# Performance work log

Hardware: AMD Instinct MI355X
Metric: run time of the kernel (lower is better)

## Reference

```python
import jax, jax.numpy as jnp
import numpy as np

NUM_HEADS = 8
NS = 27  # 3x3x3 deformable samples per query


def _resize1d(x, axis, new):
    # linear resize along one axis, align_corners=False (matches F.interpolate); identity if size matches
    old = x.shape[axis]
    if old == new:
        return x
    pos = (jnp.arange(new, dtype=jnp.float32) + 0.5) * (old / new) - 0.5
    f = jnp.floor(pos)
    w = pos - f
    i0 = jnp.clip(f, 0, old - 1).astype(jnp.int32)
    i1 = jnp.clip(f + 1, 0, old - 1).astype(jnp.int32)
    shp = [1] * x.ndim
    shp[axis] = new
    w = w.reshape(shp)
    return jnp.take(x, i0, axis=axis) * (1 - w) + jnp.take(x, i1, axis=axis) * w


def _rel_to_abs(x):
    # x: (b, d, h, w, w+NS-1) -> (b, d, h, w, NS) via the pad/reshape shifting trick
    b, d, h, w, c = x.shape
    x = jnp.pad(x, ((0, 0), (0, 0), (0, 0), (0, 0), (0, 1)))
    x = x.reshape(b, d, h, w * (c + 1))
    x = jnp.pad(x, ((0, 0), (0, 0), (0, 0), (0, NS - 1)))
    x = x.reshape(b, d, h, w + 1, NS + w - 1)
    return x[:, :, :, :w, w - 1:]


def _rel_logits_1d(q, rel_k):
    # q: (BH, 1, A, B, C, hd); rel_k: (C+NS-1, hd) -> (BH, A, B, C, NS)
    logits = jnp.einsum('nzxywd,rd->nzxywr', q, rel_k)
    n, z, a, b, c, r = logits.shape
    return _rel_to_abs(logits.reshape(n, z * a, b, c, r))


def _pos_emb(q, rel_depth, rel_height, rel_width, D, H, W):
    # q: (BH, 1, D, H, W, hd) -> (BH, D, H, W, NS)
    rw = _resize1d(rel_width, 0, W + NS - 1)
    rh = _resize1d(rel_height, 0, H + NS - 1)
    rd = _resize1d(rel_depth, 0, D + NS - 1)
    lw = _rel_logits_1d(q, rw)            # (BH, D, H, W, NS)
    qh = jnp.swapaxes(q, 3, 4)            # (BH, 1, D, W, H, hd)
    lh = _rel_logits_1d(qh, rh)           # (BH, D, W, H, NS)
    qd = jnp.swapaxes(qh, 2, 4)           # (BH, 1, H, W, D, hd)
    ld = _rel_logits_1d(qd, rd)           # (BH, H, W, D, NS)
    # trilinear resize of lh/ld to (D, H, W) over spatial axes (identity when D==H==W)
    for ax, tgt in ((1, D), (2, H), (3, W)):
        lh = _resize1d(lh, ax, tgt)
        ld = _resize1d(ld, ax, tgt)
    return lw + lh + ld


def _deform_unfold3d(x, offset):
    # x: (BH, C, D, H, W); offset: (BH, NS*3, D, H, W) -> (BH, C*NS, D*H*W)
    BH, C, D, H, W = x.shape
    off = offset.reshape(BH, NS, 3, D, H, W)
    k = jnp.arange(NS)
    kz = (k // 9 - 1).astype(jnp.float32)
    ky = (k // 3 % 3 - 1).astype(jnp.float32)
    kx = (k % 3 - 1).astype(jnp.float32)
    zz, yy, xx = jnp.meshgrid(jnp.arange(D, dtype=jnp.float32),
                              jnp.arange(H, dtype=jnp.float32),
                              jnp.arange(W, dtype=jnp.float32), indexing='ij')
    pz = zz + kz[:, None, None, None] + off[:, :, 0]   # (BH, NS, D, H, W)
    py = yy + ky[:, None, None, None] + off[:, :, 1]
    px = xx + kx[:, None, None, None] + off[:, :, 2]
    z0 = jnp.floor(pz); y0 = jnp.floor(py); x0 = jnp.floor(px)
    wz = pz - z0; wy = py - y0; wx = px - x0
    z0 = z0.astype(jnp.int32); y0 = y0.astype(jnp.int32); x0 = x0.astype(jnp.int32)
    S = D * H * W
    xf = x.reshape(BH, C, S)
    acc = jnp.zeros((BH, C, NS * S), dtype=x.dtype)
    for dz in (0, 1):
        for dy in (0, 1):
            for dx in (0, 1):
                zi = z0 + dz; yi = y0 + dy; xi = x0 + dx
                valid = ((zi >= 0) & (zi < D) & (yi >= 0) & (yi < H) & (xi >= 0) & (xi < W)).astype(x.dtype)
                w = (wz if dz else 1 - wz) * (wy if dy else 1 - wy) * (wx if dx else 1 - wx) * valid
                idx = (jnp.clip(zi, 0, D - 1) * H + jnp.clip(yi, 0, H - 1)) * W + jnp.clip(xi, 0, W - 1)
                g = jnp.take_along_axis(xf, idx.reshape(BH, 1, NS * S), axis=2)  # (BH, C, NS*S)
                acc = acc + g * w.reshape(BH, 1, NS * S)
    return acc.reshape(BH, C * NS, S)


def _forward(x, w_qkv, w_proj, b_proj, w_off, rel_depth, rel_height, rel_width, D, H, W):
    B, N, C = x.shape
    nh = NUM_HEADS
    hd = C // nh
    scale = hd ** -0.5
    BH = B * nh
    qkv = (x @ w_qkv.T).reshape(B, N, 3, nh, hd)
    q = qkv[:, :, 0].transpose(0, 2, 1, 3)  # (B, nh, N, hd)
    k = qkv[:, :, 1].transpose(0, 2, 1, 3)
    v = qkv[:, :, 2].transpose(0, 2, 1, 3)
    offset = (x.reshape(B, N, nh, hd) @ w_off.T).transpose(0, 2, 3, 1).reshape(BH, NS * 3, D, H, W)
    kmap = k.transpose(0, 1, 3, 2).reshape(BH, hd, D, H, W)
    vmap = v.transpose(0, 1, 3, 2).reshape(BH, hd, D, H, W)
    ks = _deform_unfold3d(kmap, offset).transpose(0, 2, 1).reshape(B, nh, N, hd, NS)
    vs = _deform_unfold3d(vmap, offset).reshape(B, nh, hd, NS, N).transpose(0, 1, 4, 3, 2)  # (B, nh, N, NS, hd)
    attn = jnp.einsum('bhnd,bhnds->bhns', q, ks) * scale
    pos = _pos_emb(q.reshape(BH, 1, D, H, W, hd), rel_depth, rel_height, rel_width, D, H, W).reshape(B, nh, N, NS)
    attn = jax.nn.softmax(attn + pos, axis=-1)
    out = jnp.einsum('bhns,bhnsd->bhnd', attn, vs).transpose(0, 2, 1, 3).reshape(B, N, C)
    return out @ w_proj.T + b_proj


def setup_inputs():
    key = jax.random.key(0)
    ks = jax.random.split(key, 8)
    B, D, H, W, C = 1, 16, 16, 16, 512
    N = D * H * W
    hd = C // NUM_HEADS
    return {
        'x': jax.random.normal(ks[0], (B, N, C), dtype=jnp.float32),
        'w_qkv': jax.random.normal(ks[1], (3 * C, C), dtype=jnp.float32) * 0.02,
        'w_proj': jax.random.normal(ks[2], (C, C), dtype=jnp.float32) * 0.02,
        'b_proj': jnp.zeros((C,), dtype=jnp.float32),
        'w_off': jax.random.normal(ks[3], (NS * 3, hd), dtype=jnp.float32) * 0.01,
        'rel_depth': jax.random.normal(ks[4], (D + NS - 1, hd), dtype=jnp.float32) * hd ** -0.5,
        'rel_height': jax.random.normal(ks[5], (H + NS - 1, hd), dtype=jnp.float32) * hd ** -0.5,
        'rel_width': jax.random.normal(ks[6], (W + NS - 1, hd), dtype=jnp.float32) * hd ** -0.5,
        'D': D, 'H': H, 'W': W,
    }


def reference(x, w_qkv, w_proj, b_proj, w_off, rel_depth, rel_height, rel_width, D, H, W):
    return _forward(x, w_qkv, w_proj, b_proj, w_off, rel_depth, rel_height, rel_width, D, H, W)
```

## Files before the change

kernel.cpp:

```cpp
#include <hip/hip_runtime.h>
#include <hip/hip_fp16.h>
#include <math.h>
#include <stdint.h>

#define NH    8
#define HD    64
#define NTOK  4096
#define CDIM  512
#define NSAMP 27

typedef __attribute__((ext_vector_type(8))) _Float16 half8;
typedef __attribute__((ext_vector_type(4))) float floatx4;
typedef unsigned short ushort_t;

__device__ __forceinline__ ushort_t f16b(float f) {
  return __half_as_ushort(__float2half(f));
}
__device__ __forceinline__ __half2 u2h2(uint32_t u) { return __builtin_bit_cast(__half2, u); }
__device__ __forceinline__ uint32_t h22u(__half2 h) { return __builtin_bit_cast(uint32_t, h); }

__device__ __forceinline__ float wave_sum_bcast(float x) {
#define DPP_STEP(ctrl, rmask)                                                   \
  { int t = __builtin_amdgcn_update_dpp(0, __float_as_int(x), ctrl, rmask, 0xf, \
                                        true);                                  \
    x += __int_as_float(t); }
  DPP_STEP(0x111, 0xf)
  DPP_STEP(0x112, 0xf)
  DPP_STEP(0x114, 0xf)
  DPP_STEP(0x118, 0xf)
  DPP_STEP(0x142, 0xa)
  DPP_STEP(0x143, 0xc)
#undef DPP_STEP
  return __int_as_float(__builtin_amdgcn_readlane(__float_as_int(x), 63));
}

__global__ __launch_bounds__(256) void k_cvt(const float* __restrict__ x,
                                             const float* __restrict__ wq,
                                             const float* __restrict__ wp,
                                             const float* __restrict__ w_off,
                                             const float* __restrict__ rel_d,
                                             const float* __restrict__ rel_h,
                                             const float* __restrict__ rel_w,
                                             ushort_t* __restrict__ xb,
                                             ushort_t* __restrict__ wqb,
                                             ushort_t* __restrict__ wpb,
                                             ushort_t* __restrict__ w_offh,
                                             ushort_t* __restrict__ relh) {
  int i = blockIdx.x * 256 + threadIdx.x;
  const float4* src = nullptr;
  ushort_t* dst;
  int off;
  float4 v = make_float4(0.f, 0.f, 0.f, 0.f);
  if (i < 524288)      { src = (const float4*)x;  dst = xb;  off = i; }
  else if (i < 720896) { src = (const float4*)wq; dst = wqb; off = i - 524288; }
  else if (i < 786432) { src = (const float4*)wp; dst = wpb; off = i - 720896; }
  else {
    int t = i - 786432;
    if (t < 2048) {
      off = t;
      int e = t * 4, row = e >> 6;
      if (row < 81) v = *(const float4*)&w_off[e];
      dst = w_offh;
    } else {
      off = t - 2048;
      int e = off * 4, row = e >> 6, col = e & 63;
      if (row < 42)       v = *(const float4*)&rel_w[row * 64 + col];
      else if (row < 84)  v = *(const float4*)&rel_h[(row - 42) * 64 + col];
      else if (row < 126) v = *(const float4*)&rel_d[(row - 84) * 64 + col];
      dst = relh;
    }
  }
  if (src) v = src[off];
  ushort4 o = make_ushort4(f16b(v.x), f16b(v.y), f16b(v.z), f16b(v.w));
  *(ushort4*)&dst[(size_t)off * 4] = o;
}

__global__ __launch_bounds__(256) void k_qkv(const ushort_t* __restrict__ Ah,
                                             const ushort_t* __restrict__ Bth,
                                             ushort_t* __restrict__ qh16,
                                             uint32_t* __restrict__ kvb) {
  __shared__ __align__(16) ushort_t As[128 * 32];
  __shared__ __align__(16) ushort_t Bs[128 * 32];
  __shared__ __align__(16) ushort_t Cs[128 * 136];
  const int tid = threadIdx.x;
  const int wave = tid >> 6, lane = tid & 63;
  const int wr = wave >> 1, wc = wave & 1;
  const int m15 = lane & 15, quad = lane >> 4;
  const int bm = blockIdx.x, bn = blockIdx.y;
  const bool is_q = (bn < 4);
  const int h = bn - 4;
  floatx4 acc[4][4];
#pragma unroll
  for (int i = 0; i < 4; i++)
#pragma unroll
    for (int j = 0; j < 4; j++) acc[i][j] = {0.f, 0.f, 0.f, 0.f};

  const int r0 = tid >> 2, c0 = (tid & 3) * 8;
  const int r1 = r0 + 64;
  const int brA = is_q ? (bn * 128 + r0) : (512 + h * 64 + r0);
  const int brB = is_q ? (bn * 128 + r1) : (1024 + h * 64 + r0);
  for (int k0 = 0; k0 < 512; k0 += 32) {
    *(uint4*)&As[r0 * 32 + c0] = *(const uint4*)&Ah[(size_t)(bm * 128 + r0) * 512 + k0 + c0];
    *(uint4*)&As[r1 * 32 + c0] = *(const uint4*)&Ah[(size_t)(bm * 128 + r1) * 512 + k0 + c0];
    *(uint4*)&Bs[r0 * 32 + c0] = *(const uint4*)&Bth[(size_t)brA * 512 + k0 + c0];
    *(uint4*)&Bs[r1 * 32 + c0] = *(const uint4*)&Bth[(size_t)brB * 512 + k0 + c0];
    __syncthreads();
    half8 af[4], bf[4];
#pragma unroll
    for (int i = 0; i < 4; i++)
      af[i] = *(const half8*)&As[(wr * 64 + i * 16 + m15) * 32 + quad * 8];
#pragma unroll
    for (int j = 0; j < 4; j++)
      bf[j] = *(const half8*)&Bs[(wc * 64 + j * 16 + m15) * 32 + quad * 8];
#pragma unroll
    for (int i = 0; i < 4; i++)
#pragma unroll
      for (int j = 0; j < 4; j++)
        acc[i][j] = __builtin_amdgcn_mfma_f32_16x16x32_f16(af[i], bf[j], acc[i][j], 0, 0, 0);
    __syncthreads();
  }

#pragma unroll
  for (int i = 0; i < 4; i++)
#pragma unroll
    for (int j = 0; j < 4; j++) {
      int col = wc * 64 + j * 16 + m15;
#pragma unroll
      for (int r = 0; r < 4; r++) {
        int row = wr * 64 + i * 16 + quad * 4 + r;
        Cs[row * 136 + col] = f16b(acc[i][j][r]);
      }
    }
  __syncthreads();

  if (is_q) {
#pragma unroll
    for (int it = 0; it < 8; it++) {
      int id = it * 256 + tid;
      int hh = id >> 10, row = (id >> 3) & 127, chunk = id & 7;
      uint4 d = *(const uint4*)&Cs[row * 136 + hh * 64 + chunk * 8];
      int hq = bn * 2 + hh;
      *(uint4*)&qh16[((size_t)hq * NTOK + bm * 128 + row) * 64 + chunk * 8] = d;
    }
  } else {
#pragma unroll
    for (int it = 0; it < 8; it++) {
      int id = it * 256 + tid;
      int row = id >> 4, chunk = id & 15;
      uint2 kk = *(const uint2*)&Cs[row * 136 + chunk * 4];
      uint2 vv = *(const uint2*)&Cs[row * 136 + 64 + chunk * 4];
      uint4 o;
      o.x = (kk.x & 0xffffu) | (vv.x << 16);
      o.y = (kk.x >> 16) | (vv.x & 0xffff0000u);
      o.z = (kk.y & 0xffffu) | (vv.y << 16);
      o.w = (kk.y >> 16) | (vv.y & 0xffff0000u);
      *(uint4*)&kvb[((size_t)h * NTOK + bm * 128 + row) * 64 + chunk * 4] = o;
    }
  }
}

__global__ __launch_bounds__(256) void k_aux(const ushort_t* __restrict__ xh,
                                             const ushort_t* __restrict__ qh16,
                                             const ushort_t* __restrict__ w_offh,
                                             const ushort_t* __restrict__ relh,
                                             float* __restrict__ ob,
                                             float* __restrict__ Pb) {
  __shared__ __align__(16) ushort_t As[128 * 32];
  __shared__ __align__(16) ushort_t Bs[128 * 32];
  const int tid = threadIdx.x;
  const int wave = tid >> 6, lane = tid & 63;
  const int wr = wave >> 1, wc = wave & 1;
  const int m15 = lane & 15, quad = lane >> 4;
  const int bm = blockIdx.x;
  const int mode = blockIdx.y >> 3, h = blockIdx.y & 7;

  const ushort_t* A;  int lda;
  const ushort_t* B;
  float* C;  int NC;
  if (mode == 0) { A = xh + h * 64;                  lda = 512; B = w_offh; C = ob + (size_t)h * NTOK * 81;  NC = 81; }
  else           { A = qh16 + (size_t)h * NTOK * 64; lda = 64;  B = relh;   C = Pb + (size_t)h * NTOK * 126; NC = 126; }

  floatx4 acc[4][4];
#pragma unroll
  for (int i = 0; i < 4; i++)
#pragma unroll
    for (int j = 0; j < 4; j++) acc[i][j] = {0.f, 0.f, 0.f, 0.f};

  const int r0 = tid >> 2, c0 = (tid & 3) * 8;
  const int r1 = r0 + 64;
  for (int k0 = 0; k0 < 64; k0 += 32) {
    *(uint4*)&As[r0 * 32 + c0] = *(const uint4*)&A[(size_t)(bm * 128 + r0) * lda + k0 + c0];
    *(uint4*)&As[r1 * 32 + c0] = *(const uint4*)&A[(size_t)(bm * 128 + r1) * lda + k0 + c0];
    *(uint4*)&Bs[r0 * 32 + c0] = *(const uint4*)&B[(size_t)r0 * 64 + k0 + c0];
    *(uint4*)&Bs[r1 * 32 + c0] = *(const uint4*)&B[(size_t)r1 * 64 + k0 + c0];
    __syncthreads();
    half8 af[4], bf[4];
#pragma unroll
    for (int i = 0; i < 4; i++)
      af[i] = *(const half8*)&As[(wr * 64 + i * 16 + m15) * 32 + quad * 8];
#pragma unroll
    for (int j = 0; j < 4; j++)
      bf[j] = *(const half8*)&Bs[(wc * 64 + j * 16 + m15) * 32 + quad * 8];
#pragma unroll
    for (int i = 0; i < 4; i++)
#pragma unroll
      for (int j = 0; j < 4; j++)
        acc[i][j] = __builtin_amdgcn_mfma_f32_16x16x32_f16(af[i], bf[j], acc[i][j], 0, 0, 0);
    __syncthreads();
  }

#pragma unroll
  for (int i = 0; i < 4; i++)
#pragma unroll
    for (int j = 0; j < 4; j++) {
      int col = wc * 64 + j * 16 + m15;
      if (col < NC) {
#pragma unroll
        for (int r = 0; r < 4; r++) {
          int row = bm * 128 + wr * 64 + i * 16 + quad * 4 + r;
          C[(size_t)row * NC + col] = acc[i][j][r];
        }
      }
    }
}

__global__ __launch_bounds__(256) void k_attn(const ushort_t* __restrict__ qh16,
                                              const uint32_t* __restrict__ kvb,
                                              const float* __restrict__ obuf,
                                              const float* __restrict__ Pbuf,
                                              ushort_t* __restrict__ attb16) {
  __shared__ int      s_off[4][NSAMP][8];
  __shared__ uint32_t s_cwh[4][NSAMP][8];
  __shared__ uint32_t vpair[4][14][64];
  __shared__ uint32_t s_wp[4][14];
  const int bid = blockIdx.x;
  const int h = bid & 7;
  const int wave = threadIdx.x >> 6;
  const int lane = threadIdx.x & 63;
  const int n = (bid >> 3) * 4 + wave;
  const int z = n >> 8, y = (n >> 4) & 15, xq = n & 15;
  const float qd = __half2float(__ushort_as_half(qh16[((size_t)h * NTOK + n) * 64 + lane]));
  const char* kvc = (const char*)(kvb + (size_t)h * NTOK * 64);
  const uint32_t lane4 = (uint32_t)lane * 4u;

  if (lane < NSAMP) {
    const int s = lane;
    const float* op = &obuf[((size_t)h * NTOK + n) * 81 + s * 3];
    float oz = op[0], oy = op[1], ox = op[2];
    float pz = (float)(z + (s / 9) - 1) + oz;
    float py = (float)(y + ((s / 3) % 3) - 1) + oy;
    float px = (float)(xq + (s % 3) - 1) + ox;
    float fz = floorf(pz), fy = floorf(py), fx = floorf(px);
    float wz = pz - fz, wy = py - fy, wx = px - fx;
    int z0 = (int)fz, y0 = (int)fy, x0 = (int)fx;
    int      oarr[8];
    uint32_t warr[8];
#pragma unroll
    for (int c = 0; c < 8; c++) {
      int dz = (c >> 2) & 1, dy = (c >> 1) & 1, dx = c & 1;
      int zi = z0 + dz, yi = y0 + dy, xi = x0 + dx;
      bool valid = (zi >= 0) && (zi < 16) && (yi >= 0) && (yi < 16) && (xi >= 0) && (xi < 16);
      float w = (dz ? wz : 1.f - wz) * (dy ? wy : 1.f - wy) * (dx ? wx : 1.f - wx);
      int zc = min(max(zi, 0), 15), yc = min(max(yi, 0), 15), xc = min(max(xi, 0), 15);
      oarr[c] = ((zc * 16 + yc) * 16 + xc) * 256;
      uint32_t hw = (uint32_t)f16b(valid ? w : 0.f);
      warr[c] = hw | (hw << 16);
    }
    *(int4*)&s_off[wave][s][0]  = make_int4(oarr[0], oarr[1], oarr[2], oarr[3]);
    *(int4*)&s_off[wave][s][4]  = make_int4(oarr[4], oarr[5], oarr[6], oarr[7]);
    *(uint4*)&s_cwh[wave][s][0] = make_uint4(warr[0], warr[1], warr[2], warr[3]);
    *(uint4*)&s_cwh[wave][s][4] = make_uint4(warr[4], warr[5], warr[6], warr[7]);
  }

  float mydot = 0.f;
  uint32_t prev_acc = 0;
#pragma unroll 2
  for (int s = 0; s < NSAMP; s++) {
    int4  o0 = *(const int4*)&s_off[wave][s][0];
    int4  o1 = *(const int4*)&s_off[wave][s][4];
    uint4 c0 = *(const uint4*)&s_cwh[wave][s][0];
    uint4 c1 = *(const uint4*)&s_cwh[wave][s][4];
    __half2 acc2 = u2h2(0u);
    uint32_t p;
#define CORNER(OV, WV)                                                       \
    p = *(const uint32_t*)(kvc + (uint32_t)((uint32_t)OV + lane4));          \
    acc2 = __hfma2(u2h2(WV), u2h2(p), acc2);
    CORNER(o0.x, c0.x) CORNER(o0.y, c0.y) CORNER(o0.z, c0.z) CORNER(o0.w, c0.w)
    CORNER(o1.x, c1.x) CORNER(o1.y, c1.y) CORNER(o1.z, c1.z) CORNER(o1.w, c1.w)
#undef CORNER
    float ak = __half2float(acc2.x);
    float tot = wave_sum_bcast(qd * ak);
    mydot = (lane == s) ? tot : mydot;
    uint32_t au = h22u(acc2);
    if (s & 1)
      vpair[wave][s >> 1][lane] = (prev_acc >> 16) | (au & 0xffff0000u);
    else
      prev_acc = au;
  }
  vpair[wave][13][lane] = prev_acc >> 16;

  float logit = -INFINITY;
  if (lane < NSAMP) {
    int j = 15 + lane - xq;
    int n2 = (z * 16 + xq) * 16 + y;
    int n3 = (xq * 16 + z) * 16 + y;
    float pos = Pbuf[((size_t)h * NTOK + n) * 126 + j]
              + Pbuf[((size_t)h * NTOK + n2) * 126 + 42 + j]
              + Pbuf[((size_t)h * NTOK + n3) * 126 + 84 + j];
    logit = mydot * 0.125f + pos;
  }

  float mx = logit;
#pragma unroll
  for (int off = 32; off >= 1; off >>= 1) mx = fmaxf(mx, __shfl_xor(mx, off, 64));
  float e = __expf(logit - mx);
  float sum = e;
#pragma unroll
  for (int off = 32; off >= 1; off >>= 1) sum += __shfl_xor(sum, off, 64);
  const float wgt = e / sum;
  uint32_t hw = (uint32_t)f16b(wgt);
  uint32_t nw = (uint32_t)__shfl_down((int)hw, 1, 64);
  if ((lane & 1) == 0 && lane < 28)
    s_wp[wave][lane >> 1] = hw | (nw << 16);

  __half2 out2 = u2h2(0u);
#pragma unroll
  for (int p2 = 0; p2 < 14; p2++) {
    __half2 v2 = u2h2(vpair[wave][p2][lane]);
    __half2 w2 = u2h2(s_wp[wave][p2]);
    out2 = __hfma2(w2, v2, out2);
  }
  float out = __half2float(out2.x) + __half2float(out2.y);
  attb16[(size_t)n * 512 + h * 64 + lane] = f16b(out);
}

__global__ __launch_bounds__(256) void k_proj(const ushort_t* __restrict__ Ah,
                                              const ushort_t* __restrict__ Bth,
                                              const float* __restrict__ bias,
                                              float* __restrict__ out) {
  __shared__ __align__(16) ushort_t As[128 * 32];
  __shared__ __align__(16) ushort_t Bs[128 * 32];
  const int tid = threadIdx.x;
  const int wave = tid >> 6, lane = tid & 63;
  const int wr = wave >> 1, wc = wave & 1;
  const int m15 = lane & 15, quad = lane >> 4;
  const int bm = blockIdx.x, bn = blockIdx.y;
  floatx4 acc[4][4];
#pragma unroll
  for (int i = 0; i < 4; i++)
#pragma unroll
    for (int j = 0; j < 4; j++) acc[i][j] = {0.f, 0.f, 0.f, 0.f};

  const int r0 = tid >> 2, c0 = (tid & 3) * 8;
  const int r1 = r0 + 64;
  for (int k0 = 0; k0 < 512; k0 += 32) {
    *(uint4*)&As[r0 * 32 + c0] = *(const uint4*)&Ah[(size_t)(bm * 128 + r0) * 512 + k0 + c0];
    *(uint4*)&As[r1 * 32 + c0] = *(const uint4*)&Ah[(size_t)(bm * 128 + r1) * 512 + k0 + c0];
    *(uint4*)&Bs[r0 * 32 + c0] = *(const uint4*)&Bth[(size_t)(bn * 128 + r0) * 512 + k0 + c0];
    *(uint4*)&Bs[r1 * 32 + c0] = *(const uint4*)&Bth[(size_t)(bn * 128 + r1) * 512 + k0 + c0];
    __syncthreads();
    half8 af[4], bf[4];
#pragma unroll
    for (int i = 0; i < 4; i++)
      af[i] = *(const half8*)&As[(wr * 64 + i * 16 + m15) * 32 + quad * 8];
#pragma unroll
    for (int j = 0; j < 4; j++)
      bf[j] = *(const half8*)&Bs[(wc * 64 + j * 16 + m15) * 32 + quad * 8];
#pragma unroll
    for (int i = 0; i < 4; i++)
#pragma unroll
      for (int j = 0; j < 4; j++)
        acc[i][j] = __builtin_amdgcn_mfma_f32_16x16x32_f16(af[i], bf[j], acc[i][j], 0, 0, 0);
    __syncthreads();
  }

#pragma unroll
  for (int i = 0; i < 4; i++)
#pragma unroll
    for (int j = 0; j < 4; j++) {
      int col = bn * 128 + wc * 64 + j * 16 + m15;
      float b = bias[col];
#pragma unroll
      for (int r = 0; r < 4; r++) {
        int row = bm * 128 + wr * 64 + i * 16 + quad * 4 + r;
        out[(size_t)row * 512 + col] = acc[i][j][r] + b;
      }
    }
}

extern "C" void kernel_launch(void* const* d_in, const int* in_sizes, int n_in,
                              void* d_out, int out_size, void* d_ws, size_t ws_size,
                              hipStream_t stream) {
  const float* x      = (const float*)d_in[0];
  const float* w_qkv  = (const float*)d_in[1];
  const float* w_proj = (const float*)d_in[2];
  const float* b_proj = (const float*)d_in[3];
  const float* w_off  = (const float*)d_in[4];
  const float* rel_d  = (const float*)d_in[5];
  const float* rel_h  = (const float*)d_in[6];
  const float* rel_w  = (const float*)d_in[7];

  char* ws = (char*)d_ws;
  uint32_t* kvb    = (uint32_t*)ws; ws += (size_t)NH * NTOK * 64 * 4;
  float*    ob     = (float*)ws;    ws += (size_t)NH * NTOK * 81 * 4;
  float*    Pb     = (float*)ws;    ws += (size_t)NH * NTOK * 126 * 4;
  ushort_t* attb16 = (ushort_t*)ws; ws += (size_t)NTOK * CDIM * 2;
  ushort_t* xh     = (ushort_t*)ws; ws += (size_t)NTOK * CDIM * 2;
  ushort_t* wqh    = (ushort_t*)ws; ws += (size_t)3 * CDIM * CDIM * 2;
  ushort_t* wph    = (ushort_t*)ws; ws += (size_t)CDIM * CDIM * 2;
  ushort_t* qh16   = (ushort_t*)ws; ws += (size_t)NH * NTOK * 64 * 2;
  ushort_t* w_offh = (ushort_t*)ws; ws += (size_t)128 * 64 * 2;
  ushort_t* relh   = (ushort_t*)ws; ws += (size_t)128 * 64 * 2;
  float*    out    = (float*)d_out;

  k_cvt <<<dim3(3088), dim3(256), 0, stream>>>(x, w_qkv, w_proj, w_off, rel_d, rel_h,
                                               rel_w, xh, wqh, wph, w_offh, relh);
  k_qkv <<<dim3(32, 12), dim3(256), 0, stream>>>(xh, wqh, qh16, kvb);
  k_aux <<<dim3(32, 16), dim3(256), 0, stream>>>(xh, qh16, w_offh, relh, ob, Pb);
  k_attn<<<dim3(8192),   dim3(256), 0, stream>>>(qh16, kvb, ob, Pb, attb16);
  k_proj<<<dim3(32, 4),  dim3(256), 0, stream>>>(attb16, wph, b_proj, out);
}
```

Measured before the change: 181.6 us.

## Fold offset and relative-position projections into the QKV GEMM via precomposed weights

Precomputes block-diagonal offset weights and rel-embedding×Wq composite weights so the offset and positional logits come straight from x. They are computed in one larger merged GEMM launch alongside QKV, and the separate aux kernel that depended on q is removed. This drops one dependent launch and lets the small GEMMs share the QKV grid. In exchange the offset and rel GEMMs now use K=512 instead of 64, which adds MFMA work and weight traffic. The composite weights are rounded to fp16 after an fp32 product, which changes numerics slightly.

After: 194.6 us. +7.2%, slower.

```diff
diff --git a/kernel.cpp b/kernel.cpp
--- a/kernel.cpp
+++ b/kernel.cpp
@@ -34,51 +34,73 @@
   return __int_as_float(__builtin_amdgcn_readlane(__float_as_int(x), 63));
 }
 
-__global__ __launch_bounds__(256) void k_cvt(const float* __restrict__ x,
-                                             const float* __restrict__ wq,
-                                             const float* __restrict__ wp,
-                                             const float* __restrict__ w_off,
-                                             const float* __restrict__ rel_d,
-                                             const float* __restrict__ rel_h,
-                                             const float* __restrict__ rel_w,
+__global__ __launch_bounds__(256) void k_cvt(const float4* __restrict__ x,
+                                             const float4* __restrict__ wq,
+                                             const float4* __restrict__ wp,
                                              ushort_t* __restrict__ xb,
                                              ushort_t* __restrict__ wqb,
-                                             ushort_t* __restrict__ wpb,
-                                             ushort_t* __restrict__ w_offh,
-                                             ushort_t* __restrict__ relh) {
+                                             ushort_t* __restrict__ wpb) {
   int i = blockIdx.x * 256 + threadIdx.x;
-  const float4* src = nullptr;
-  ushort_t* dst;
-  int off;
-  float4 v = make_float4(0.f, 0.f, 0.f, 0.f);
-  if (i < 524288)      { src = (const float4*)x;  dst = xb;  off = i; }
-  else if (i < 720896) { src = (const float4*)wq; dst = wqb; off = i - 524288; }
-  else if (i < 786432) { src = (const float4*)wp; dst = wpb; off = i - 720896; }
-  else {
-    int t = i - 786432;
-    if (t < 2048) {
-      off = t;
-      int e = t * 4, row = e >> 6;
-      if (row < 81) v = *(const float4*)&w_off[e];
-      dst = w_offh;
-    } else {
-      off = t - 2048;
-      int e = off * 4, row = e >> 6, col = e & 63;
-      if (row < 42)       v = *(const float4*)&rel_w[row * 64 + col];
-      else if (row < 84)  v = *(const float4*)&rel_h[(row - 42) * 64 + col];
-      else if (row < 126) v = *(const float4*)&rel_d[(row - 84) * 64 + col];
-      dst = relh;
-    }
-  }
-  if (src) v = src[off];
+  const float4* src; ushort_t* dst; int off;
+  if (i < 524288)      { src = x;  dst = xb;  off = i; }
+  else if (i < 720896) { src = wq; dst = wqb; off = i - 524288; }
+  else                 { src = wp; dst = wpb; off = i - 720896; }
+  float4 v = src[off];
   ushort4 o = make_ushort4(f16b(v.x), f16b(v.y), f16b(v.z), f16b(v.w));
   *(ushort4*)&dst[(size_t)off * 4] = o;
 }
 
-__global__ __launch_bounds__(256) void k_qkv(const ushort_t* __restrict__ Ah,
-                                             const ushort_t* __restrict__ Bth,
-                                             ushort_t* __restrict__ qh16,
-                                             uint32_t* __restrict__ kvb) {
+__global__ __launch_bounds__(256) void k_wpre(const float* __restrict__ w_qkv,
+                                              const float* __restrict__ w_off,
+                                              const float* __restrict__ rel_d,
+                                              const float* __restrict__ rel_h,
+                                              const float* __restrict__ rel_w,
+                                              ushort_t* __restrict__ woffd,
+                                              ushort_t* __restrict__ wrelall) {
+  const int b = blockIdx.x, tid = threadIdx.x;
+  if (b < 384) {
+    int i = b * 256 + tid;
+    int e = i * 4;
+    int r = e >> 9, K = e & 511;
+    float4 v = make_float4(0.f, 0.f, 0.f, 0.f);
+    if (r < 648) {
+      int h = r / 81, j = r - h * 81;
+      int kb = K - h * 64;
+      if (kb >= 0 && kb < 64) v = *(const float4*)&w_off[j * 64 + kb];
+    }
+    ushort4 o = make_ushort4(f16b(v.x), f16b(v.y), f16b(v.z), f16b(v.w));
+    *(ushort4*)&woffd[(size_t)e] = o;
+  } else {
+    int row = b - 384;
+    ushort_t* dst = wrelall + (size_t)row * 512;
+    if (row >= 1008) { dst[tid] = 0; dst[tid + 256] = 0; return; }
+    int h = row / 126, j = row - h * 126;
+    const float* relrow = (j < 42) ? (rel_w + j * 64)
+                        : (j < 84) ? (rel_h + (j - 42) * 64)
+                                   : (rel_d + (j - 84) * 64);
+    __shared__ float rl[64];
+    if (tid < 64) rl[tid] = relrow[tid];
+    __syncthreads();
+    float a0 = 0.f, a1 = 0.f;
+#pragma unroll 8
+    for (int d = 0; d < 64; d++) {
+      const float* wr = &w_qkv[(size_t)(h * 64 + d) * 512];
+      a0 = fmaf(rl[d], wr[tid], a0);
+      a1 = fmaf(rl[d], wr[tid + 256], a1);
+    }
+    dst[tid] = f16b(a0);
+    dst[tid + 256] = f16b(a1);
+  }
+}
+
+__global__ __launch_bounds__(256) void k_mega(const ushort_t* __restrict__ Ah,
+                                              const ushort_t* __restrict__ wqh,
+                                              const ushort_t* __restrict__ woffd,
+                                              const ushort_t* __restrict__ wrelall,
+                                              ushort_t* __restrict__ qh16,
+                                              uint32_t* __restrict__ kvb,
+                                              float* __restrict__ ob,
+                                              float* __restrict__ Pb) {
   __shared__ __align__(16) ushort_t As[128 * 32];
   __shared__ __align__(16) ushort_t Bs[128 * 32];
   __shared__ __align__(16) ushort_t Cs[128 * 136];
@@ -87,8 +109,6 @@
   const int wr = wave >> 1, wc = wave & 1;
   const int m15 = lane & 15, quad = lane >> 4;
   const int bm = blockIdx.x, bn = blockIdx.y;
-  const bool is_q = (bn < 4);
-  const int h = bn - 4;
   floatx4 acc[4][4];
 #pragma unroll
   for (int i = 0; i < 4; i++)
@@ -97,13 +117,18 @@
 
   const int r0 = tid >> 2, c0 = (tid & 3) * 8;
   const int r1 = r0 + 64;
-  const int brA = is_q ? (bn * 128 + r0) : (512 + h * 64 + r0);
-  const int brB = is_q ? (bn * 128 + r1) : (1024 + h * 64 + r0);
+  const ushort_t* Bp;
+  int baseA, baseB;
+  if (bn < 4)       { Bp = wqh;     baseA = bn * 128 + r0;            baseB = bn * 128 + r1; }
+  else if (bn < 12) { Bp = wqh;     baseA = 512 + (bn - 4) * 64 + r0; baseB = 1024 + (bn - 4) * 64 + r0; }
+  else if (bn < 18) { Bp = woffd;   baseA = (bn - 12) * 128 + r0;     baseB = (bn - 12) * 128 + r1; }
+  else              { Bp = wrelall; baseA = (bn - 18) * 128 + r0;     baseB = (bn - 18) * 128 + r1; }
+
   for (int k0 = 0; k0 < 512; k0 += 32) {
     *(uint4*)&As[r0 * 32 + c0] = *(const uint4*)&Ah[(size_t)(bm * 128 + r0) * 512 + k0 + c0];
     *(uint4*)&As[r1 * 32 + c0] = *(const uint4*)&Ah[(size_t)(bm * 128 + r1) * 512 + k0 + c0];
-    *(uint4*)&Bs[r0 * 32 + c0] = *(const uint4*)&Bth[(size_t)brA * 512 + k0 + c0];
-    *(uint4*)&Bs[r1 * 32 + c0] = *(const uint4*)&Bth[(size_t)brB * 512 + k0 + c0];
+    *(uint4*)&Bs[r0 * 32 + c0] = *(const uint4*)&Bp[(size_t)baseA * 512 + k0 + c0];
+    *(uint4*)&Bs[r1 * 32 + c0] = *(const uint4*)&Bp[(size_t)baseB * 512 + k0 + c0];
     __syncthreads();
     half8 af[4], bf[4];
 #pragma unroll
@@ -120,108 +145,77 @@
     __syncthreads();
   }
 
-#pragma unroll
-  for (int i = 0; i < 4; i++)
-#pragma unroll
-    for (int j = 0; j < 4; j++) {
-      int col = wc * 64 + j * 16 + m15;
-#pragma unroll
-      for (int r = 0; r < 4; r++) {
-        int row = wr * 64 + i * 16 + quad * 4 + r;
-        Cs[row * 136 + col] = f16b(acc[i][j][r]);
+  if (bn < 12) {
+#pragma unroll
+    for (int i = 0; i < 4; i++)
+#pragma unroll
+      for (int j = 0; j < 4; j++) {
+        int col = wc * 64 + j * 16 + m15;
+#pragma unroll
+        for (int r = 0; r < 4; r++) {
+          int row = wr * 64 + i * 16 + quad * 4 + r;
+          Cs[row * 136 + col] = f16b(acc[i][j][r]);
+        }
+      }
+    __syncthreads();
+    if (bn < 4) {
+#pragma unroll
+      for (int it = 0; it < 8; it++) {
+        int id = it * 256 + tid;
+        int hh = id >> 10, row = (id >> 3) & 127, chunk = id & 7;
+        uint4 d = *(const uint4*)&Cs[row * 136 + hh * 64 + chunk * 8];
+        int hq = bn * 2 + hh;
+        *(uint4*)&qh16[((size_t)hq * NTOK + bm * 128 + row) * 64 + chunk * 8] = d;
+      }
+    } else {
+      const int h = bn - 4;
+#pragma unroll
+      for (int it = 0; it < 8; it++) {
+        int id = it * 256 + tid;
+        int row = id >> 4, chunk = id & 15;
+        uint2 kk = *(const uint2*)&Cs[row * 136 + chunk * 4];
+        uint2 vv = *(const uint2*)&Cs[row * 136 + 64 + chunk * 4];
+        uint4 o;
+        o.x = (kk.x & 0xffffu) | (vv.x << 16);
+        o.y = (kk.x >> 16) | (vv.x & 0xffff0000u);
+        o.z = (kk.y & 0xffffu) | (vv.y << 16);
+        o.w = (kk.y >> 16) | (vv.y & 0xffff0000u);
+        *(uint4*)&kvb[((size_t)h * NTOK + bm * 128 + row) * 64 + chunk * 4] = o;
       }
     }
-  __syncthreads();
-
-  if (is_q) {
-#pragma unroll
-    for (int it = 0; it < 8; it++) {
-      int id = it * 256 + tid;
-      int hh = id >> 10, row = (id >> 3) & 127, chunk = id & 7;
-      uint4 d = *(const uint4*)&Cs[row * 136 + hh * 64 + chunk * 8];
-      int hq = bn * 2 + hh;
-      *(uint4*)&qh16[((size_t)hq * NTOK + bm * 128 + row) * 64 + chunk * 8] = d;
-    }
+  } else if (bn < 18) {
+    const int cbase = (bn - 12) * 128;
+#pragma unroll
+    for (int i = 0; i < 4; i++)
+#pragma unroll
+      for (int j = 0; j < 4; j++) {
+        int col = cbase + wc * 64 + j * 16 + m15;
+        if (col < 648) {
+          int h = col / 81, j81 = col - h * 81;
+#pragma unroll
+          for (int r = 0; r < 4; r++) {
+            int row = bm * 128 + wr * 64 + i * 16 + quad * 4 + r;
+            ob[((size_t)h * NTOK + row) * 81 + j81] = acc[i][j][r];
+          }
+        }
+      }
   } else {
-#pragma unroll
-    for (int it = 0; it < 8; it++) {
-      int id = it * 256 + tid;
-      int row = id >> 4, chunk = id & 15;
-      uint2 kk = *(const uint2*)&Cs[row * 136 + chunk * 4];
-      uint2 vv = *(const uint2*)&Cs[row * 136 + 64 + chunk * 4];
-      uint4 o;
-      o.x = (kk.x & 0xffffu) | (vv.x << 16);
-      o.y = (kk.x >> 16) | (vv.x & 0xffff0000u);
-      o.z = (kk.y & 0xffffu) | (vv.y << 16);
-      o.w = (kk.y >> 16) | (vv.y & 0xffff0000u);
-      *(uint4*)&kvb[((size_t)h * NTOK + bm * 128 + row) * 64 + chunk * 4] = o;
-    }
-  }
-}
-
-__global__ __launch_bounds__(256) void k_aux(const ushort_t* __restrict__ xh,
-                                             const ushort_t* __restrict__ qh16,
-                                             const ushort_t* __restrict__ w_offh,
-                                             const ushort_t* __restrict__ relh,
-                                             float* __restrict__ ob,
-                                             float* __restrict__ Pb) {
-  __shared__ __align__(16) ushort_t As[128 * 32];
-  __shared__ __align__(16) ushort_t Bs[128 * 32];
-  const int tid = threadIdx.x;
-  const int wave = tid >> 6, lane = tid & 63;
-  const int wr = wave >> 1, wc = wave & 1;
-  const int m15 = lane & 15, quad = lane >> 4;
-  const int bm = blockIdx.x;
-  const int mode = blockIdx.y >> 3, h = blockIdx.y & 7;
-
-  const ushort_t* A;  int lda;
-  const ushort_t* B;
-  float* C;  int NC;
-  if (mode == 0) { A = xh + h * 64;                  lda = 512; B = w_offh; C = ob + (size_t)h * NTOK * 81;  NC = 81; }
-  else           { A = qh16 + (size_t)h * NTOK * 64; lda = 64;  B = relh;   C = Pb + (size_t)h * NTOK * 126; NC = 126; }
-
-  floatx4 acc[4][4];
-#pragma unroll
-  for (int i = 0; i < 4; i++)
-#pragma unroll
-    for (int j = 0; j < 4; j++) acc[i][j] = {0.f, 0.f, 0.f, 0.f};
-
-  const int r0 = tid >> 2, c0 = (tid & 3) * 8;
-  const int r1 = r0 + 64;
-  for (int k0 = 0; k0 < 64; k0 += 32) {
-    *(uint4*)&As[r0 * 32 + c0] = *(const uint4*)&A[(size_t)(bm * 128 + r0) * lda + k0 + c0];
-    *(uint4*)&As[r1 * 32 + c0] = *(const uint4*)&A[(size_t)(bm * 128 + r1) * lda + k0 + c0];
-    *(uint4*)&Bs[r0 * 32 + c0] = *(const uint4*)&B[(size_t)r0 * 64 + k0 + c0];
-    *(uint4*)&Bs[r1 * 32 + c0] = *(const uint4*)&B[(size_t)r1 * 64 + k0 + c0];
-    __syncthreads();
-    half8 af[4], bf[4];
-#pragma unroll
-    for (int i = 0; i < 4; i++)
-      af[i] = *(const half8*)&As[(wr * 64 + i * 16 + m15) * 32 + quad * 8];
-#pragma unroll
-    for (int j = 0; j < 4; j++)
-      bf[j] = *(const half8*)&Bs[(wc * 64 + j * 16 + m15) * 32 + quad * 8];
-#pragma unroll
-    for (int i = 0; i < 4; i++)
-#pragma unroll
-      for (int j = 0; j < 4; j++)
-        acc[i][j] = __builtin_amdgcn_mfma_f32_16x16x32_f16(af[i], bf[j], acc[i][j], 0, 0, 0);
-    __syncthreads();
-  }
-
-#pragma unroll
-  for (int i = 0; i < 4; i++)
-#pragma unroll
-    for (int j = 0; j < 4; j++) {
-      int col = wc * 64 + j * 16 + m15;
-      if (col < NC) {
-#pragma unroll
-        for (int r = 0; r < 4; r++) {
-          int row = bm * 128 + wr * 64 + i * 16 + quad * 4 + r;
-          C[(size_t)row * NC + col] = acc[i][j][r];
+    const int cbase = (bn - 18) * 128;
+#pragma unroll
+    for (int i = 0; i < 4; i++)
+#pragma unroll
+      for (int j = 0; j < 4; j++) {
+        int col = cbase + wc * 64 + j * 16 + m15;
+        if (col < 1008) {
+          int h = col / 126, jj = col - h * 126;
+#pragma unroll
+          for (int r = 0; r < 4; r++) {
+            int row = bm * 128 + wr * 64 + i * 16 + quad * 4 + r;
+            Pb[((size_t)h * NTOK + row) * 126 + jj] = acc[i][j][r];
+          }
         }
       }
-    }
+  }
 }
 
 __global__ __launch_bounds__(256) void k_attn(const ushort_t* __restrict__ qh16,
@@ -401,22 +395,24 @@
   const float* rel_w  = (const float*)d_in[7];
 
   char* ws = (char*)d_ws;
-  uint32_t* kvb    = (uint32_t*)ws; ws += (size_t)NH * NTOK * 64 * 4;
-  float*    ob     = (float*)ws;    ws += (size_t)NH * NTOK * 81 * 4;
-  float*    Pb     = (float*)ws;    ws += (size_t)NH * NTOK * 126 * 4;
-  ushort_t* attb16 = (ushort_t*)ws; ws += (size_t)NTOK * CDIM * 2;
-  ushort_t* xh     = (ushort_t*)ws; ws += (size_t)NTOK * CDIM * 2;
-  ushort_t* wqh    = (ushort_t*)ws; ws += (size_t)3 * CDIM * CDIM * 2;
-  ushort_t* wph    = (ushort_t*)ws; ws += (size_t)CDIM * CDIM * 2;
-  ushort_t* qh16   = (ushort_t*)ws; ws += (size_t)NH * NTOK * 64 * 2;
-  ushort_t* w_offh = (ushort_t*)ws; ws += (size_t)128 * 64 * 2;
-  ushort_t* relh   = (ushort_t*)ws; ws += (size_t)128 * 64 * 2;
-  float*    out    = (float*)d_out;
-
-  k_cvt <<<dim3(3088), dim3(256), 0, stream>>>(x, w_qkv, w_proj, w_off, rel_d, rel_h,
-                                               rel_w, xh, wqh, wph, w_offh, relh);
-  k_qkv <<<dim3(32, 12), dim3(256), 0, stream>>>(xh, wqh, qh16, kvb);
-  k_aux <<<dim3(32, 16), dim3(256), 0, stream>>>(xh, qh16, w_offh, relh, ob, Pb);
-  k_attn<<<dim3(8192),   dim3(256), 0, stream>>>(qh16, kvb, ob, Pb, attb16);
-  k_proj<<<dim3(32, 4),  dim3(256), 0, stream>>>(attb16, wph, b_proj, out);
-}
+  uint32_t* kvb     = (uint32_t*)ws; ws += (size_t)NH * NTOK * 64 * 4;
+  float*    ob      = (float*)ws;    ws += (size_t)NH * NTOK * 81 * 4;
+  float*    Pb      = (float*)ws;    ws += (size_t)NH * NTOK * 126 * 4;
+  ushort_t* attb16  = (ushort_t*)ws; ws += (size_t)NTOK * CDIM * 2;
+  ushort_t* xh      = (ushort_t*)ws; ws += (size_t)NTOK * CDIM * 2;
+  ushort_t* wqh     = (ushort_t*)ws; ws += (size_t)3 * CDIM * CDIM * 2;
+  ushort_t* wph     = (ushort_t*)ws; ws += (size_t)CDIM * CDIM * 2;
+  ushort_t* qh16    = (ushort_t*)ws; ws += (size_t)NH * NTOK * 64 * 2;
+  ushort_t* woffd   = (ushort_t*)ws; ws += (size_t)768 * 512 * 2;
+  ushort_t* wrelall = (ushort_t*)ws; ws += (size_t)1024 * 512 * 2;
+  float*    out     = (float*)d_out;
+
+  k_cvt <<<dim3(3072), dim3(256), 0, stream>>>((const float4*)x, (const float4*)w_qkv,
+                                               (const float4*)w_proj, xh, wqh, wph);
+  k_wpre<<<dim3(1408), dim3(256), 0, stream>>>(w_qkv, w_off, rel_d, rel_h, rel_w,
+                                               woffd, wrelall);
+  k_mega<<<dim3(32, 26), dim3(256), 0, stream>>>(xh, wqh, woffd, wrelall,
+                                                 qh16, kvb, ob, Pb);
+  k_attn<<<dim3(8192),  dim3(256), 0, stream>>>(qh16, kvb, ob, Pb, attb16);
+  k_proj<<<dim3(32, 4), dim3(256), 0, stream>>>(attb16, wph, b_proj, out);
+}
```
